# Kernel optimization log

Measured on AMD Instinct MI355X. Metric: run time of the kernel, lower is better.

The kernel has to match this reference:

```python
import jax, jax.numpy as jnp
import numpy as np
from jax import lax

CONF_T = 0.25   # NMS.conf
IOU_T = 0.45    # NMS.iou
MAX_DET = 1000  # NMS.max_det
K_PRE = 1024    # fixed pre-NMS candidate count (static-shape surrogate for boolean filtering)
MAX_WH = 4096.0 # class offset for class-aware NMS (yolov5 trick)


def _xywh2xyxy(b):
    xy, wh = b[..., :2], b[..., 2:4]
    return jnp.concatenate([xy - wh * 0.5, xy + wh * 0.5], axis=-1)


def _box_iou(a, b):
    # a: [K,4], b: [K,4] xyxy -> [K,K]
    area_a = (a[:, 2] - a[:, 0]) * (a[:, 3] - a[:, 1])
    area_b = (b[:, 2] - b[:, 0]) * (b[:, 3] - b[:, 1])
    lt = jnp.maximum(a[:, None, :2], b[None, :, :2])
    rb = jnp.minimum(a[:, None, 2:], b[None, :, 2:])
    wh = jnp.clip(rb - lt, 0.0)
    inter = wh[..., 0] * wh[..., 1]
    return inter / (area_a[:, None] + area_b[None, :] - inter + 1e-7)


def _nms_single(p):
    # p: [N, 5+nc]
    obj = p[:, 4]
    cls_scores = p[:, 5:] * obj[:, None]          # conf = obj_conf * cls_conf
    conf = jnp.max(cls_scores, axis=-1)           # best-class confidence
    cls = jnp.argmax(cls_scores, axis=-1)
    valid = (obj > CONF_T) & (conf > CONF_T)      # candidate + conf threshold
    score = jnp.where(valid, conf, -1.0)

    top_conf, top_idx = lax.top_k(score, K_PRE)   # static pre-NMS selection
    boxes = _xywh2xyxy(p[:, :4])[top_idx]         # [K,4]
    cls_k = cls[top_idx].astype(p.dtype)
    off_boxes = boxes + (cls_k * MAX_WH)[:, None] # class-aware offset

    iou = _box_iou(off_boxes, off_boxes)          # [K,K]
    keep0 = top_conf > 0.0
    ar = jnp.arange(K_PRE)

    def body(i, keep):
        sup = (iou[i] > IOU_T) & (ar > i) & keep[i]
        return keep & ~sup

    keep = lax.fori_loop(0, K_PRE, body, keep0)

    kscore = jnp.where(keep, top_conf, -1.0)
    out_c, out_i = lax.top_k(kscore, MAX_DET)     # max_det cap
    dets = jnp.concatenate(
        [boxes[out_i], top_conf[out_i][:, None], cls_k[out_i][:, None]], axis=-1
    )                                             # [max_det, 6] (xyxy, conf, cls)
    vmask = out_c > 0.0
    dets = jnp.where(vmask[:, None], dets, 0.0)
    return dets, vmask


def setup_inputs() -> dict:
    key = jax.random.key(0)
    B, N, C = 16, 25200, 85
    x = jax.random.uniform(key, (B, N, C), dtype=jnp.float32)
    x = x.at[..., :4].multiply(640.0)  # xywh in pixel scale
    return {"x": x}


def reference(x):
    dets, vmask = jax.vmap(_nms_single)(x)
    return dets, vmask
```

## Files before the change

kernel.cpp:

```cpp
#include <hip/hip_runtime.h>
#include <cstdint>
#include <cstddef>

#define BATCH 16
#define NBOX 25200
#define NCH 85
#define KPRE 1024
#define MAXDET 1000
#define NCAND_MAX 4096
#define CSHIFT 12
#define HB 4096
#define HBASE 0x40800
#define IDX_PAD 0xFFFFFFFFu

__device__ __forceinline__ unsigned key_of(float s) {
    unsigned u = __float_as_uint(s);
    unsigned m = (u & 0x80000000u) ? ~u : (u | 0x80000000u);
    return ~m;
}

__global__ __launch_bounds__(256) void score_kernel(const float* __restrict__ x,
                                                    unsigned* __restrict__ k32) {
    int gid = blockIdx.x * 256 + threadIdx.x;
    int box = gid >> 2;
    int q = gid & 3;
    const float* rowp = x + (size_t)box * NCH;

    float obj = rowp[4];
    const float4* p4 = (const float4*)rowp;
    float4 r0 = p4[q];
    float4 r1 = p4[q + 4];
    float4 r2 = p4[q + 8];
    float4 r3 = p4[q + 12];
    float4 r4 = p4[q + 16];
    float4 rt = p4[20];
    float c79 = rowp[84];

    if (q == 0) { r0.x = -1e30f; r0.y = -1e30f; r0.z = -1e30f; r0.w = -1e30f; }
    if (q == 1) { r0.x = -1e30f; }

    float v = fmaxf(fmaxf(r0.x, r0.y), fmaxf(r0.z, r0.w));
    v = fmaxf(v, fmaxf(fmaxf(r1.x, r1.y), fmaxf(r1.z, r1.w)));
    v = fmaxf(v, fmaxf(fmaxf(r2.x, r2.y), fmaxf(r2.z, r2.w)));
    v = fmaxf(v, fmaxf(fmaxf(r3.x, r3.y), fmaxf(r3.z, r3.w)));
    v = fmaxf(v, fmaxf(fmaxf(r4.x, r4.y), fmaxf(r4.z, r4.w)));
    v = fmaxf(v, fmaxf(fmaxf(rt.x, rt.y), fmaxf(rt.z, rt.w)));
    v = fmaxf(v, c79);
    v = fmaxf(v, __shfl_xor(v, 1));
    v = fmaxf(v, __shfl_xor(v, 2));

    if (q == 0) {
        float conf = obj * v;
        bool validb = (obj > 0.25f) && (conf > 0.25f);
        k32[box] = key_of(validb ? conf : -1.0f);
    }
}

__global__ __launch_bounds__(1024) void sort_gather(const unsigned* __restrict__ k32,
                                                    float* __restrict__ topconf,
                                                    unsigned* __restrict__ topidx) {
    __shared__ unsigned long long keys[NCAND_MAX];
    __shared__ unsigned h[HB];
    __shared__ unsigned part[1024];
    __shared__ unsigned wsum[16];
    __shared__ unsigned cnt[25][16];
    __shared__ unsigned waveOff[25][16];
    __shared__ unsigned chunkBase[25];
    __shared__ unsigned totc[25];
    __shared__ unsigned cutP, nTot;
    int b = blockIdx.x, t = threadIdx.x;
    int lane = t & 63, wv = t >> 6;
    const unsigned* kb = k32 + (size_t)b * NBOX;

    unsigned kreg[25];
    unsigned validbits = 0;
    #pragma unroll
    for (int c = 0; c < 25; c++) {
        int i = c * 1024 + t;
        unsigned k = 0x80000000u;
        if (i < NBOX) k = kb[i];
        kreg[c] = k;
        validbits |= (((int)k >= 0) ? 1u : 0u) << c;
    }

    #pragma unroll
    for (int j = 0; j < HB / 1024; j++) h[t + j * 1024] = 0;
    __syncthreads();
    #pragma unroll
    for (int c = 0; c < 25; c++) {
        if ((validbits >> c) & 1u) {
            int bu = (int)(kreg[c] >> CSHIFT) - HBASE;
            bu = bu < 0 ? 0 : (bu > HB - 1 ? HB - 1 : bu);
            atomicAdd(&h[bu], 1u);
        }
    }
    __syncthreads();

    {
        unsigned s = h[4 * t] + h[4 * t + 1] + h[4 * t + 2] + h[4 * t + 3];
        part[t] = s;
        unsigned ws = s;
        #pragma unroll
        for (int off = 1; off < 64; off <<= 1) ws += __shfl_xor(ws, off);
        if (lane == 0) wsum[wv] = ws;
    }
    __syncthreads();
    if (t == 0) {
        unsigned cum = 0; int W = -1;
        for (int w = 0; w < 16; w++)
            if (W < 0) { if (cum + wsum[w] >= KPRE) W = w; else cum += wsum[w]; }
        int T = -1;
        if (W >= 0)
            for (int i = 0; i < 64; i++)
                if (T < 0) { int p = W * 64 + i; if (cum + part[p] >= KPRE) T = p; else cum += part[p]; }
        unsigned P = HB - 1;
        if (T >= 0)
            for (int j = 0; j < 4; j++) { cum += h[T * 4 + j]; if (cum >= KPRE) { P = (unsigned)(T * 4 + j); break; } }
        cutP = P + HBASE;
    }
    __syncthreads();
    unsigned P = cutP;

    unsigned passbits = 0;
    #pragma unroll
    for (int c = 0; c < 25; c++) {
        bool p = ((validbits >> c) & 1u) && ((kreg[c] >> CSHIFT) <= P);
        passbits |= (p ? 1u : 0u) << c;
    }
    #pragma unroll
    for (int c = 0; c < 25; c++) {
        unsigned long long m = __ballot((passbits >> c) & 1u);
        if (lane == 0) cnt[c][wv] = (unsigned)__popcll(m);
    }
    __syncthreads();
    if (t < 25) {
        unsigned run = 0;
        #pragma unroll
        for (int w2 = 0; w2 < 16; w2++) { waveOff[t][w2] = run; run += cnt[t][w2]; }
        totc[t] = run;
    }
    __syncthreads();
    if (t == 0) {
        unsigned acc = 0;
        for (int c = 0; c < 25; c++) { chunkBase[c] = acc; acc += totc[c]; }
        nTot = acc;
    }
    __syncthreads();
    int n = (int)nTot; if (n > NCAND_MAX) n = NCAND_MAX;
    #pragma unroll
    for (int c = 0; c < 25; c++) {
        unsigned long long m = __ballot((passbits >> c) & 1u);
        if ((passbits >> c) & 1u) {
            unsigned rank = chunkBase[c] + waveOff[c][wv] +
                            (unsigned)__popcll(lane ? (m & ((~0ull) >> (64 - lane))) : 0ull);
            if (rank < NCAND_MAX)
                keys[rank] = ((unsigned long long)kreg[c] << 32) | (unsigned)(c * 1024 + t);
        }
    }
    int m2 = KPRE;
    while (m2 < n) m2 <<= 1;
    int nq = m2 >> 10;
    for (int q = 0; q < nq; q++) { int s2 = t + (q << 10); if (s2 >= n) keys[s2] = ~0ull; }
    __syncthreads();

    for (int k = 2; k <= m2; k <<= 1) {
        for (int j = k >> 1; j > 0; j >>= 1) {
            for (int q = 0; q < nq; q++) {
                int i = t + (q << 10);
                int ixj = i ^ j;
                if (ixj > i) {
                    unsigned long long a = keys[i], bb = keys[ixj];
                    bool up = ((i & k) == 0);
                    if ((a > bb) == up) { keys[i] = bb; keys[ixj] = a; }
                }
            }
            __syncthreads();
        }
    }

    int o = (b << 10) + t;
    if (t < n) {
        unsigned long long key = keys[t];
        unsigned kk = (unsigned)(key >> 32);
        unsigned mm = ~kk;
        unsigned bits = (mm & 0x80000000u) ? (mm & 0x7FFFFFFFu) : ~mm;
        topconf[o] = __uint_as_float(bits);
        topidx[o] = (unsigned)(key & 0xFFFFFFFFu);
    } else {
        topconf[o] = -1.0f;
        topidx[o] = IDX_PAD;
    }
}

__global__ __launch_bounds__(256) void argmax_gather(const float* __restrict__ x,
                                                     const unsigned* __restrict__ topidx,
                                                     float4* __restrict__ topbox,
                                                     float4* __restrict__ topoff,
                                                     float* __restrict__ topcls) {
#pragma clang fp contract(off)
    int gid = blockIdx.x * 256 + threadIdx.x;
    int o = gid >> 2;
    int q = gid & 3;
    int b = o >> 10;
    unsigned idx = topidx[o];

    float4 box = make_float4(0.f, 0.f, 0.f, 0.f);
    float clsf = 0.f;
    if (idx != IDX_PAD) {
        size_t base = ((size_t)b * NBOX + idx) * NCH;
        float obj = x[base + 4];
        int cbase = 5 + q * 20;
        float v = -1e30f; int c = 0;
        #pragma unroll
        for (int j = 0; j < 20; j++) {
            float s = x[base + cbase + j] * obj;
            if (s > v) { v = s; c = q * 20 + j; }
        }
        #pragma unroll
        for (int off = 1; off <= 2; off <<= 1) {
            float ov = __shfl_xor(v, off);
            int   oc = __shfl_xor(c, off);
            if (ov > v || (ov == v && oc < c)) { v = ov; c = oc; }
        }
        if (q == 0) {
            float cx = x[base + 0], cy = x[base + 1], w = x[base + 2], h = x[base + 3];
            box = make_float4(cx - w * 0.5f, cy - h * 0.5f, cx + w * 0.5f, cy + h * 0.5f);
            clsf = (float)c;
        }
    }
    if (q == 0) {
        topbox[o] = box;
        topcls[o] = clsf;
        float off = clsf * 4096.0f;
        topoff[o] = make_float4(box.x + off, box.y + off, box.z + off, box.w + off);
    }
}

__global__ __launch_bounds__(256) void iou_mask(const float4* __restrict__ topoff,
                                                unsigned long long* __restrict__ mask,
                                                unsigned short* __restrict__ summ) {
#pragma clang fp contract(off)
    __shared__ float4 soff[KPRE];
    int b = blockIdx.x >> 6;
    int blk = blockIdx.x & 63;
    int t = threadIdx.x;
    for (int q = 0; q < 4; q++) {
        int u = t + q * 256;
        int s = ((u & 15) << 6) | (u >> 4);
        soff[u] = topoff[(b << 10) + s];
    }
    __syncthreads();
    int i = (blk << 4) + (t >> 4);
    int w = t & 15;
    unsigned long long bits = 0;
    int jbase = w << 6;
    if (jbase + 63 > i) {
        float4 a = soff[((i & 63) << 4) | (i >> 6)];
        float area_a = (a.z - a.x) * (a.w - a.y);
        for (int jj = 0; jj < 64; jj++) {
            int j = jbase + jj;
            float4 bb = soff[(jj << 4) | w];
            float area_b = (bb.z - bb.x) * (bb.w - bb.y);
            float ltx = fmaxf(a.x, bb.x), lty = fmaxf(a.y, bb.y);
            float rbx = fminf(a.z, bb.z), rby = fminf(a.w, bb.w);
            float wx = fmaxf(rbx - ltx, 0.0f), wy = fmaxf(rby - lty, 0.0f);
            float inter = wx * wy;
            float iou = inter / (area_a + area_b - inter + 1e-7f);
            if (j > i && iou > 0.45f) bits |= (1ull << jj);
        }
    }
    mask[((size_t)((b << 10) + i) << 4) + w] = bits;
    unsigned long long bal = __ballot(bits != 0ull);
    if (w == 0) {
        int l = t & 63;
        summ[(b << 10) + i] = (unsigned short)((bal >> ((l >> 4) << 4)) & 0xFFFFull);
    }
}

__global__ __launch_bounds__(1024) void nms_finalize(const unsigned long long* __restrict__ mask,
                                                     const unsigned short* __restrict__ summ,
                                                     const float* __restrict__ topconf,
                                                     const float4* __restrict__ topbox,
                                                     const float* __restrict__ topcls,
                                                     float* __restrict__ dets,
                                                     float* __restrict__ vmask) {
    __shared__ unsigned long long kb[16];
    int b = blockIdx.x, tid = threadIdx.x;

    if (tid < 64) {
        int lane = tid;
        const unsigned long long* mrow = mask + ((size_t)b << 14);
        unsigned long long keep0[16];
        #pragma unroll
        for (int c = 0; c < 16; c++) {
            float cf = topconf[(b << 10) + (c << 6) + lane];
            keep0[c] = __ballot(cf > 0.0f);
        }
        unsigned nz[16];
        #pragma unroll
        for (int t = 0; t < 16; t++)
            nz[t] = (unsigned)summ[(b << 10) + (t << 6) + lane];
        unsigned long long diag[16];
        #pragma unroll
        for (int t = 0; t < 16; t++)
            diag[t] = mrow[((size_t)((t << 6) + lane) << 4) + t];

        unsigned long long remv[16];
        #pragma unroll
        for (int t = 0; t < 16; t++) remv[t] = 0;

        #pragma unroll
        for (int t = 0; t < 16; t++) {
            unsigned long long live = keep0[t] & ~remv[t];
            unsigned long long kept = live;
            unsigned long long pend = live & __ballot((nz[t] >> t) & 1u);
            while (pend) {
                int j = (int)__ffsll(pend) - 1;
                pend &= pend - 1;
                if ((kept >> j) & 1ull) {
                    unsigned long long dj = __shfl(diag[t], j);
                    kept &= ~dj;
                    pend &= ~dj;
                }
            }
            if (lane == 0) kb[t] = kept;

            #pragma unroll
            for (int w = 0; w < 16; w++) {
                if (w > t) {
                    unsigned long long wm = kept & __ballot((nz[t] >> w) & 1u);
                    while (wm) {
                        int j = (int)__ffsll(wm) - 1;
                        wm &= wm - 1;
                        remv[w] |= mrow[((size_t)((t << 6) + j) << 4) + w];
                    }
                }
            }
        }
    }
    __syncthreads();

    int r = tid;
    int w = r >> 6, l = r & 63;
    unsigned long long word = kb[w];
    int keep = (int)((word >> l) & 1ull);
    int base = 0, total = 0;
    #pragma unroll
    for (int q = 0; q < 16; q++) {
        int c = __popcll(kb[q]);
        total += c;
        if (q < w) base += c;
    }
    int rank = base + __popcll((l == 0) ? 0ull : (word & ((~0ull) >> (64 - l))));
    float* drow = dets + (size_t)b * (MAXDET * 6);
    float* vm = vmask + (size_t)b * MAXDET;
    if (r < MAXDET && r >= total) {
#pragma unroll
        for (int cc = 0; cc < 6; cc++) drow[r * 6 + cc] = 0.0f;
        vm[r] = 0.0f;
    }
    if (keep && rank < MAXDET) {
        int o = (b << 10) + r;
        float4 bx = topbox[o];
        drow[rank * 6 + 0] = bx.x;
        drow[rank * 6 + 1] = bx.y;
        drow[rank * 6 + 2] = bx.z;
        drow[rank * 6 + 3] = bx.w;
        drow[rank * 6 + 4] = topconf[o];
        drow[rank * 6 + 5] = topcls[o];
        vm[rank] = 1.0f;
    }
}

extern "C" void kernel_launch(void* const* d_in, const int* in_sizes, int n_in,
                              void* d_out, int out_size, void* d_ws, size_t ws_size,
                              hipStream_t stream) {
    const float* x = (const float*)d_in[0];
    char* w = (char*)d_ws;

    unsigned long long* mask    = (unsigned long long*)(w + 0);
    unsigned*           k32     = (unsigned*)(w + 2097152);
    float4*             topbox  = (float4*)(w + 3709952);
    float4*             topoff  = (float4*)(w + 3972096);
    float*              topconf = (float*)(w + 4234240);
    float*              topcls  = (float*)(w + 4299776);
    unsigned*           topidx  = (unsigned*)(w + 4365312);
    unsigned short*     summ    = (unsigned short*)(w + 4430848);
    if (ws_size < 4463616) return;

    score_kernel<<<(BATCH * NBOX * 4) / 256, 256, 0, stream>>>(x, k32);
    sort_gather<<<BATCH, 1024, 0, stream>>>(k32, topconf, topidx);
    argmax_gather<<<(BATCH * KPRE * 4) / 256, 256, 0, stream>>>(x, topidx, topbox, topoff, topcls);
    iou_mask<<<BATCH * 64, 256, 0, stream>>>(topoff, mask, summ);

    float* dets = (float*)d_out;
    float* vmask = dets + (size_t)BATCH * MAXDET * 6;
    nms_finalize<<<BATCH, 1024, 0, stream>>>(mask, summ, topconf, topbox, topcls, dets, vmask);
}
```

Measured before the change: 104.4 us.

## Use wavefront shuffles for intra-wave bitonic sort stages in top-k

Replaces the shared-memory bitonic sort with a hybrid for the 2048-element case. Each thread keeps its two elements in registers and runs the compare-exchange steps with stride below 64 through __shfl_xor inside a wavefront. Only strides of 64 and above go through LDS with __syncthreads. This removes most of the block-wide barriers and LDS round trips, at the cost of always sorting at least 2048 elements even when the candidate count is at most 1024.

After: 95.57 us. -8.4%, faster.

```diff
diff --git a/kernel.cpp b/kernel.cpp
--- a/kernel.cpp
+++ b/kernel.cpp
@@ -157,35 +157,81 @@
                 keys[rank] = ((unsigned long long)kreg[c] << 32) | (unsigned)(c * 1024 + t);
         }
     }
-    int m2 = KPRE;
+    int m2 = 2048;
     while (m2 < n) m2 <<= 1;
     int nq = m2 >> 10;
     for (int q = 0; q < nq; q++) { int s2 = t + (q << 10); if (s2 >= n) keys[s2] = ~0ull; }
     __syncthreads();
 
-    for (int k = 2; k <= m2; k <<= 1) {
-        for (int j = k >> 1; j > 0; j >>= 1) {
-            for (int q = 0; q < nq; q++) {
-                int i = t + (q << 10);
-                int ixj = i ^ j;
-                if (ixj > i) {
-                    unsigned long long a = keys[i], bb = keys[ixj];
-                    bool up = ((i & k) == 0);
-                    if ((a > bb) == up) { keys[i] = bb; keys[ixj] = a; }
+    unsigned long long myKey;
+    if (m2 == 2048) {
+        const int i0 = t, i1 = t + 1024;
+        unsigned long long e0 = keys[i0], e1 = keys[i1];
+        #pragma unroll
+        for (int k = 2; k <= 64; k <<= 1) {
+            #pragma unroll
+            for (int j = k >> 1; j > 0; j >>= 1) {
+                unsigned long long p0 = __shfl_xor(e0, j);
+                unsigned long long p1 = __shfl_xor(e1, j);
+                bool sel0 = ((i0 & k) == 0) != ((i0 & j) != 0);
+                bool sel1 = ((i1 & k) == 0) != ((i1 & j) != 0);
+                e0 = sel0 ? (e0 < p0 ? e0 : p0) : (e0 > p0 ? e0 : p0);
+                e1 = sel1 ? (e1 < p1 ? e1 : p1) : (e1 > p1 ? e1 : p1);
+            }
+        }
+        for (int k = 128; k <= 2048; k <<= 1) {
+            keys[i0] = e0; keys[i1] = e1;
+            __syncthreads();
+            for (int j = k >> 1; j >= 64; j >>= 1) {
+                #pragma unroll
+                for (int q = 0; q < 2; q++) {
+                    int i = t + (q << 10);
+                    int ixj = i ^ j;
+                    if (ixj > i) {
+                        unsigned long long a = keys[i], bb2 = keys[ixj];
+                        bool up = ((i & k) == 0);
+                        if ((a > bb2) == up) { keys[i] = bb2; keys[ixj] = a; }
+                    }
                 }
-            }
-            __syncthreads();
-        }
+                __syncthreads();
+            }
+            e0 = keys[i0]; e1 = keys[i1];
+            #pragma unroll
+            for (int j = 32; j > 0; j >>= 1) {
+                unsigned long long p0 = __shfl_xor(e0, j);
+                unsigned long long p1 = __shfl_xor(e1, j);
+                bool sel0 = ((i0 & k) == 0) != ((i0 & j) != 0);
+                bool sel1 = ((i1 & k) == 0) != ((i1 & j) != 0);
+                e0 = sel0 ? (e0 < p0 ? e0 : p0) : (e0 > p0 ? e0 : p0);
+                e1 = sel1 ? (e1 < p1 ? e1 : p1) : (e1 > p1 ? e1 : p1);
+            }
+        }
+        myKey = e0;
+    } else {
+        for (int k = 2; k <= m2; k <<= 1) {
+            for (int j = k >> 1; j > 0; j >>= 1) {
+                for (int q = 0; q < nq; q++) {
+                    int i = t + (q << 10);
+                    int ixj = i ^ j;
+                    if (ixj > i) {
+                        unsigned long long a = keys[i], bb2 = keys[ixj];
+                        bool up = ((i & k) == 0);
+                        if ((a > bb2) == up) { keys[i] = bb2; keys[ixj] = a; }
+                    }
+                }
+                __syncthreads();
+            }
+        }
+        myKey = keys[t];
     }
 
     int o = (b << 10) + t;
     if (t < n) {
-        unsigned long long key = keys[t];
-        unsigned kk = (unsigned)(key >> 32);
+        unsigned kk = (unsigned)(myKey >> 32);
         unsigned mm = ~kk;
         unsigned bits = (mm & 0x80000000u) ? (mm & 0x7FFFFFFFu) : ~mm;
         topconf[o] = __uint_as_float(bits);
-        topidx[o] = (unsigned)(key & 0xFFFFFFFFu);
+        topidx[o] = (unsigned)(myKey & 0xFFFFFFFFu);
     } else {
         topconf[o] = -1.0f;
         topidx[o] = IDX_PAD;
```
